# Optimization experiments

Hardware: AMD Instinct MI355X
Metric: run time of the kernel (lower is better)

The kernel has to match this reference:

```python
import jax, jax.numpy as jnp
import numpy as np

H = 56; W = 56; WS = 7; SS = 3; HEADS = 12; DIM = 384
N = WS * WS; NW = (H // WS) * (W // WS); EPS = 1e-5


def _attn_mask():
    img = np.zeros((H, W), np.float32)
    cnt = 0
    for hs in (slice(0, -WS), slice(-WS, -SS), slice(-SS, None)):
        for ws in (slice(0, -WS), slice(-WS, -SS), slice(-SS, None)):
            img[hs, ws] = cnt
            cnt += 1
    m = img.reshape(H // WS, WS, W // WS, WS).transpose(0, 2, 1, 3).reshape(-1, N)
    d = m[:, None, :] - m[:, :, None]
    return jnp.asarray(np.where(d != 0, -100.0, 0.0).astype(np.float32))


def _rel_coords():
    c = np.stack(np.meshgrid(np.arange(WS), np.arange(WS), indexing='ij')).reshape(2, -1)
    rel = (c[:, :, None] - c[:, None, :]).astype(np.float32)
    rel = np.sign(rel) * np.log1p(np.abs(rel))
    return jnp.asarray(np.stack([rel[0], rel[1]], -1).reshape(-1, 2))


ATTN_MASK = _attn_mask()  # (NW, N, N)
REL = _rel_coords()       # (N*N, 2)


def _ln(x, g, b):
    mu = x.mean(-1, keepdims=True)
    var = ((x - mu) ** 2).mean(-1, keepdims=True)
    return (x - mu) / jnp.sqrt(var + EPS) * g + b


def setup_inputs() -> dict:
    key = jax.random.key(0)
    ks = jax.random.split(key, 8)
    s = 0.02
    B = 32
    return {
        'x': jax.random.normal(ks[0], (B, H * W, DIM), jnp.float32),
        'norm1_g': jnp.ones((DIM,), jnp.float32),
        'norm1_b': jnp.zeros((DIM,), jnp.float32),
        'qkv_w': jax.random.normal(ks[1], (DIM, 3 * DIM), jnp.float32) * s,
        'qkv_b': jnp.zeros((3 * DIM,), jnp.float32),
        'tau': jnp.ones((HEADS,), jnp.float32),
        'proj_w': jax.random.normal(ks[2], (DIM, DIM), jnp.float32) * s,
        'proj_b': jnp.zeros((DIM,), jnp.float32),
        'crpb_w1': jax.random.normal(ks[3], (2, 64), jnp.float32) * s,
        'crpb_b1': jnp.zeros((64,), jnp.float32),
        'crpb_w2': jax.random.normal(ks[4], (64, HEADS), jnp.float32) * s,
        'crpb_b2': jnp.zeros((HEADS,), jnp.float32),
        'norm2_g': jnp.ones((DIM,), jnp.float32),
        'norm2_b': jnp.zeros((DIM,), jnp.float32),
        'mlp_w1': jax.random.normal(ks[5], (DIM, 4 * DIM), jnp.float32) * s,
        'mlp_b1': jnp.zeros((4 * DIM,), jnp.float32),
        'mlp_w2': jax.random.normal(ks[6], (4 * DIM, DIM), jnp.float32) * s,
        'mlp_b2': jnp.zeros((DIM,), jnp.float32),
    }


def reference(x, norm1_g, norm1_b, qkv_w, qkv_b, tau, proj_w, proj_b,
              crpb_w1, crpb_b1, crpb_w2, crpb_b2, norm2_g, norm2_b,
              mlp_w1, mlp_b1, mlp_w2, mlp_b2):
    B = x.shape[0]
    shortcut = x
    h = _ln(x, norm1_g, norm1_b).reshape(B, H, W, DIM)
    # cyclic shift
    h = jnp.roll(h, (-SS, -SS), axis=(1, 2))
    # window partition -> (B*NW, N, DIM)
    xw = h.reshape(B, H // WS, WS, W // WS, WS, DIM).transpose(0, 1, 3, 2, 4, 5).reshape(-1, N, DIM)
    qkv = xw @ qkv_w + qkv_b
    q, k, v = jnp.split(qkv, 3, axis=-1)
    hd = DIM // HEADS
    def to_heads(t):
        return t.reshape(-1, N, HEADS, hd).transpose(0, 2, 1, 3)  # (Bw, heads, N, hd)
    q, k, v = to_heads(q), to_heads(k), to_heads(v)
    q = q / jnp.maximum(jnp.linalg.norm(q, axis=-1, keepdims=True), 1e-12)
    k = k / jnp.maximum(jnp.linalg.norm(k, axis=-1, keepdims=True), 1e-12)
    attn = jnp.einsum('whnd,whmd->whnm', q, k) * tau[None, :, None, None]
    # continuous relative position bias
    bias = jax.nn.relu(REL @ crpb_w1 + crpb_b1) @ crpb_w2 + crpb_b2  # (N*N, heads)
    bias = bias.reshape(N, N, HEADS).transpose(2, 0, 1)
    attn = attn + bias[None]
    attn = attn.reshape(B, NW, HEADS, N, N) + ATTN_MASK[None, :, None]
    attn = jax.nn.softmax(attn.reshape(-1, HEADS, N, N), axis=-1)
    out = jnp.einsum('whnm,whmd->whnd', attn, v).transpose(0, 2, 1, 3).reshape(-1, N, DIM)
    out = out @ proj_w + proj_b
    # window reverse
    h = out.reshape(B, H // WS, W // WS, WS, WS, DIM).transpose(0, 1, 3, 2, 4, 5).reshape(B, H, W, DIM)
    h = jnp.roll(h, (SS, SS), axis=(1, 2)).reshape(B, H * W, DIM)
    x = shortcut + h
    m = _ln(x, norm2_g, norm2_b)
    m = jax.nn.gelu(m @ mlp_w1 + mlp_b1, approximate=False) @ mlp_w2 + mlp_b2
    return x + m
```

## Files before the change

kernel.cpp:

```cpp
#include <hip/hip_runtime.h>
#include <cstdint>
#include <cstddef>


typedef unsigned short u16;
typedef __bf16 bf16x8 __attribute__((ext_vector_type(8)));
typedef float f32x4 __attribute__((ext_vector_type(4)));

__device__ __forceinline__ u16 f2bf(float f) {
  unsigned u = __builtin_bit_cast(unsigned, f);
  u += 0x7fffu + ((u >> 16) & 1u);
  return (u16)(u >> 16);
}

__device__ __forceinline__ void gll16(const u16* g, u16* l) {
  __builtin_amdgcn_global_load_lds(
      (const __attribute__((address_space(1))) void*)g,
      (__attribute__((address_space(3))) void*)l, 16, 0, 0);
}

__device__ __forceinline__ bf16x8 ldfrag(const u16* rowp, int l4) {
  return *(const bf16x8*)(rowp + 8 * l4);
}

__global__ __launch_bounds__(256) void fill_k(float* o, int n) {
  int i = blockIdx.x * 256 + threadIdx.x;
  if (i < n) o[i] = 12345.0f;
}

__global__ __launch_bounds__(256) void wconv_k(
    const float* __restrict__ qkv_w, const float* __restrict__ proj_w,
    const float* __restrict__ mlp_w1, const float* __restrict__ mlp_w2,
    u16* __restrict__ o) {
  const int id = blockIdx.x * 256 + threadIdx.x;
  if (id < 442368) {
    const int n = id / 384, k = id - n * 384;
    o[id] = f2bf(qkv_w[k * 1152 + n]);
  } else if (id < 589824) {
    const int e = id - 442368; const int n = e / 384, k = e - n * 384;
    o[id] = f2bf(proj_w[k * 384 + n]);
  } else if (id < 1179648) {
    const int e = id - 589824; const int n = e / 384, k = e - n * 384;
    o[id] = f2bf(mlp_w1[k * 1536 + n]);
  } else {
    const int e = id - 1179648; const int n = e / 1536, k = e - n * 1536;
    o[id] = f2bf(mlp_w2[k * 384 + n]);
  }
}

__global__ __launch_bounds__(256) void biastab_k(
    const float* __restrict__ w1, const float* __restrict__ b1,
    const float* __restrict__ w2, const float* __restrict__ b2,
    float* __restrict__ biasT) {
  const int id = blockIdx.x * 256 + threadIdx.x;
  if (id >= 2401) return;
  const int i = id / 49, j = id - i * 49;
  const int r1 = i / 7, c1 = i - r1 * 7, r2 = j / 7, c2 = j - r2 * 7;
  float dy = (float)(r1 - r2), dx = (float)(c1 - c2);
  dy = copysignf(log1pf(fabsf(dy)), dy);
  dx = copysignf(log1pf(fabsf(dx)), dx);
  float accv[12];
#pragma unroll
  for (int t = 0; t < 12; ++t) accv[t] = b2[t];
  for (int u = 0; u < 64; ++u) {
    float hu = fmaxf(dy * w1[u] + dx * w1[64 + u] + b1[u], 0.0f);
#pragma unroll
    for (int t = 0; t < 12; ++t) accv[t] += hu * w2[u * 12 + t];
  }
#pragma unroll
  for (int t = 0; t < 12; ++t) biasT[t * 2401 + id] = accv[t];
}

template <int WINMAP>
__global__ __launch_bounds__(256, 4) void ln_k(
    const float* __restrict__ X, const float* __restrict__ g,
    const float* __restrict__ b, u16* __restrict__ O) {
  const int t = blockIdx.x * 4 + (threadIdx.x >> 6);
  const int lane = threadIdx.x & 63;
  const float* xr = X + (size_t)t * 384;
  float v[6];
  float s = 0.f;
#pragma unroll
  for (int i = 0; i < 6; ++i) { v[i] = xr[lane + i * 64]; s += v[i]; }
#pragma unroll
  for (int m = 1; m < 64; m <<= 1) s += __shfl_xor(s, m);
  const float mu = s * (1.0f / 384.0f);
  float q = 0.f;
#pragma unroll
  for (int i = 0; i < 6; ++i) { float d = v[i] - mu; q += d * d; }
#pragma unroll
  for (int m = 1; m < 64; m <<= 1) q += __shfl_xor(q, m);
  const float rstd = rsqrtf(q * (1.0f / 384.0f) + 1e-5f);
  size_t row;
  if constexpr (WINMAP) {
    const int bb = t / 3136, hw = t - bb * 3136;
    const int ho = hw / 56, wo = hw - ho * 56;
    int hs = ho - 3; if (hs < 0) hs += 56;
    int ws2 = wo - 3; if (ws2 < 0) ws2 += 56;
    const int h7 = hs / 7, w7 = ws2 / 7;
    const int wwin = bb * 64 + h7 * 8 + w7;
    const int p = (hs - h7 * 7) * 7 + (ws2 - w7 * 7);
    row = (size_t)wwin * 49 + p;
  } else {
    row = (size_t)t;
  }
  u16* orow = O + row * 384;
#pragma unroll
  for (int i = 0; i < 6; ++i) {
    const int d = lane + i * 64;
    orow[d] = f2bf((v[i] - mu) * rstd * g[d] + b[d]);
  }
}

template <int EPI>
__global__ __launch_bounds__(256, 2) void gemm_k(
    const u16* __restrict__ A, const u16* __restrict__ Bt,
    const float* __restrict__ bias, const float* __restrict__ aux,
    void* __restrict__ outp, int M, int N, int K) {
  __shared__ u16 Ash[128 * 32];
  __shared__ u16 Bsh[128 * 32];
  const int tid = threadIdx.x;
  const int lane = tid & 63;
  const int wv = tid >> 6;
  const int wrow = wv >> 1, wcol = wv & 1;
  const int l15 = lane & 15, l4 = lane >> 4;

  const int nx = gridDim.x;
  const int nwg = nx * gridDim.y;
  int bid = blockIdx.y * nx + blockIdx.x;
  bid = (bid & 7) * (nwg >> 3) + (bid >> 3);
  const int tileN = (bid % nx) * 128;
  const int tileM = (bid / nx) * 128;

  f32x4 acc[4][4] = {};

  const int r0 = wv * 16 + (lane >> 2);
  const int c0 = (lane & 3) * 8;
  const u16* Ag = A + (size_t)(tileM + r0) * K + c0;
  const u16* Bg = Bt + (size_t)(tileN + r0) * K + c0;
  const size_t rowskip = (size_t)64 * K;
  u16* Al0 = &Ash[wv * 512];
  u16* Al1 = &Ash[(4 + wv) * 512];
  u16* Bl0 = &Bsh[wv * 512];
  u16* Bl1 = &Bsh[(4 + wv) * 512];

  for (int k0 = 0; k0 < K; k0 += 32) {
    __syncthreads();
    gll16(Ag + k0, Al0);
    gll16(Ag + rowskip + k0, Al1);
    gll16(Bg + k0, Bl0);
    gll16(Bg + rowskip + k0, Bl1);
    __syncthreads();
    bf16x8 af[4], bfr[4];
#pragma unroll
    for (int f = 0; f < 4; ++f) {
      af[f] = ldfrag(&Ash[(wrow * 64 + f * 16 + l15) * 32], l4);
      bfr[f] = ldfrag(&Bsh[(wcol * 64 + f * 16 + l15) * 32], l4);
    }
#pragma unroll
    for (int fm = 0; fm < 4; ++fm)
#pragma unroll
      for (int fn = 0; fn < 4; ++fn)
        acc[fm][fn] = __builtin_amdgcn_mfma_f32_16x16x32_bf16(
            af[fm], bfr[fn], acc[fm][fn], 0, 0, 0);
  }

  const int baseRow = tileM + wrow * 64;
  const int baseCol = tileN + wcol * 64;

  if constexpr (EPI == 0) {
    u16* O = (u16*)outp;
#pragma unroll
    for (int fm = 0; fm < 4; ++fm) {
#pragma unroll
      for (int hp = 0; hp < 2; ++hp) {
        const int c0e = baseCol + hp * 32;
        const int seg = c0e >> 5;
        const bool nrm = seg < 24;
        const float tfac = (seg < 12) ? aux[seg] : 1.0f;
        const float b0 = bias[c0e + l15];
        const float b1 = bias[c0e + 16 + l15];
#pragma unroll
        for (int r = 0; r < 4; ++r) {
          float v0 = acc[fm][2 * hp][r] + b0;
          float v1 = acc[fm][2 * hp + 1][r] + b1;
          if (nrm) {
            float ss = v0 * v0 + v1 * v1;
            ss += __shfl_xor(ss, 1);
            ss += __shfl_xor(ss, 2);
            ss += __shfl_xor(ss, 4);
            ss += __shfl_xor(ss, 8);
            const float f = tfac / fmaxf(sqrtf(ss), 1e-12f);
            v0 *= f; v1 *= f;
          }
          const size_t row = (size_t)(baseRow + fm * 16 + l4 * 4 + r);
          O[row * N + c0e + l15] = f2bf(v0);
          O[row * N + c0e + 16 + l15] = f2bf(v1);
        }
      }
    }
  } else if constexpr (EPI == 1) {
    float* O = (float*)outp;
    const float* X = aux;
#pragma unroll
    for (int fm = 0; fm < 4; ++fm) {
#pragma unroll
      for (int r = 0; r < 4; ++r) {
        const int row = baseRow + fm * 16 + l4 * 4 + r;
        const int w = row / 49, p = row - w * 49;
        const int bb = w >> 6, widx = w & 63;
        const int p7 = p / 7;
        int hs = (widx >> 3) * 7 + p7;
        int ws2 = (widx & 7) * 7 + (p - p7 * 7);
        int ho = hs + 3; if (ho >= 56) ho -= 56;
        int wo = ws2 + 3; if (wo >= 56) wo -= 56;
        const size_t tok = (size_t)bb * 3136 + ho * 56 + wo;
#pragma unroll
        for (int fn = 0; fn < 4; ++fn) {
          const int col = baseCol + fn * 16 + l15;
          O[tok * 384 + col] = X[tok * 384 + col] + acc[fm][fn][r] + bias[col];
        }
      }
    }
  } else if constexpr (EPI == 2) {
    u16* O = (u16*)outp;
#pragma unroll
    for (int fm = 0; fm < 4; ++fm) {
#pragma unroll
      for (int fn = 0; fn < 4; ++fn) {
        const int col = baseCol + fn * 16 + l15;
        const float bc = bias[col];
#pragma unroll
        for (int r = 0; r < 4; ++r) {
          const size_t row = (size_t)(baseRow + fm * 16 + l4 * 4 + r);
          const float v = acc[fm][fn][r] + bc;
          const float g = 0.5f * v * (1.0f + erff(v * 0.70710678118654752f));
          O[row * N + col] = f2bf(g);
        }
      }
    }
  } else {
    float* O = (float*)outp;
#pragma unroll
    for (int fm = 0; fm < 4; ++fm) {
#pragma unroll
      for (int fn = 0; fn < 4; ++fn) {
        const int col = baseCol + fn * 16 + l15;
        const float bc = bias[col];
#pragma unroll
        for (int r = 0; r < 4; ++r) {
          const size_t row = (size_t)(baseRow + fm * 16 + l4 * 4 + r);
          O[row * N + col] += acc[fm][fn][r] + bc;
        }
      }
    }
  }
}

__global__ __launch_bounds__(256, 2) void attn_k(
    const u16* __restrict__ qkv, const float* __restrict__ biasT,
    u16* __restrict__ outp) {
  __shared__ u16 lds[4][7552];
  const int tid = threadIdx.x, lane = tid & 63, wid = tid >> 6;
  const int l15 = lane & 15, l4 = lane >> 4;
  const int W = blockIdx.x * 4 + wid;
  const int w = W / 12, h = W - w * 12;
  u16* S = lds[wid];
  u16* Q = S;
  u16* Kl = S + 2560;
  u16* P = S;
  u16* VT = S + 5120;
  float* sums = (float*)(S + 7424);
  const u16* base = qkv + (size_t)w * 56448 + h * 32;
  const int widx = w & 63, wh = widx >> 3, ww = widx & 7;
  const bool masked = (wh == 7) || (ww == 7);

#pragma unroll
  for (int it = 0; it < 4; ++it) {
    const int row = it * 16 + (lane >> 2);
    const int c8 = (lane & 3) * 8;
    uint4 qv = {0, 0, 0, 0}, kv = {0, 0, 0, 0};
    if (row < 49) {
      qv = *(const uint4*)(base + (size_t)row * 1152 + c8);
      kv = *(const uint4*)(base + (size_t)row * 1152 + 384 + c8);
    }
    *(uint4*)&Q[row * 40 + c8] = qv;
    *(uint4*)&Kl[row * 40 + c8] = kv;
  }
  {
    const int d = lane & 31;
    const int jh = lane >> 5;
#pragma unroll 4
    for (int jt = 0; jt < 32; ++jt) {
      const int j = jt * 2 + jh;
      u16 val = 0;
      if (j < 49) val = base[(size_t)j * 1152 + 768 + d];
      VT[d * 72 + j] = val;
    }
  }
  __syncthreads();

  f32x4 sc[4][4] = {};
  {
    bf16x8 aq[4], bk[4];
#pragma unroll
    for (int f = 0; f < 4; ++f) aq[f] = ldfrag(&Q[(f * 16 + l15) * 40], l4);
#pragma unroll
    for (int f = 0; f < 4; ++f) bk[f] = ldfrag(&Kl[(f * 16 + l15) * 40], l4);
#pragma unroll
    for (int fm = 0; fm < 4; ++fm)
#pragma unroll
      for (int fn = 0; fn < 4; ++fn)
        sc[fm][fn] = __builtin_amdgcn_mfma_f32_16x16x32_bf16(
            aq[fm], bk[fn], sc[fm][fn], 0, 0, 0);
  }
  __syncthreads();

  int codej[4] = {0, 0, 0, 0};
  if (masked) {
#pragma unroll
    for (int fn = 0; fn < 4; ++fn) {
      const int j = fn * 16 + l15;
      const int pr = j / 7, pc = j - pr * 7;
      const int rr2 = (wh == 7) ? ((pr < 4) ? 1 : 2) : 0;
      const int cc2 = (ww == 7) ? ((pc < 4) ? 1 : 2) : 0;
      codej[fn] = rr2 * 3 + cc2;
    }
  }
#pragma unroll
  for (int fm = 0; fm < 4; ++fm) {
#pragma unroll
    for (int r = 0; r < 4; ++r) {
      const int i = fm * 16 + l4 * 4 + r;
      const bool iok = i < 49;
      int ci = 0;
      if (masked && iok) {
        const int pr = i / 7, pc = i - pr * 7;
        const int rr2 = (wh == 7) ? ((pr < 4) ? 1 : 2) : 0;
        const int cc2 = (ww == 7) ? ((pc < 4) ? 1 : 2) : 0;
        ci = rr2 * 3 + cc2;
      }
      const float* brow = biasT + (size_t)h * 2401 + (iok ? i : 0) * 49;
      float sv[4];
#pragma unroll
      for (int fn = 0; fn < 4; ++fn) {
        const int j = fn * 16 + l15;
        float s = sc[fm][fn][r];
        if (iok && j < 49) {
          s += brow[j];
          if (masked && codej[fn] != ci) s -= 100.0f;
        } else {
          s = -1e30f;
        }
        sv[fn] = s;
      }
      float mx = fmaxf(fmaxf(sv[0], sv[1]), fmaxf(sv[2], sv[3]));
      mx = fmaxf(mx, __shfl_xor(mx, 1));
      mx = fmaxf(mx, __shfl_xor(mx, 2));
      mx = fmaxf(mx, __shfl_xor(mx, 4));
      mx = fmaxf(mx, __shfl_xor(mx, 8));
      float sm = 0.f;
      u16 pb[4];
#pragma unroll
      for (int fn = 0; fn < 4; ++fn) {
        const float e = __expf(sv[fn] - mx);
        sm += e;
        pb[fn] = f2bf(e);
      }
      sm += __shfl_xor(sm, 1);
      sm += __shfl_xor(sm, 2);
      sm += __shfl_xor(sm, 4);
      sm += __shfl_xor(sm, 8);
#pragma unroll
      for (int fn = 0; fn < 4; ++fn) P[i * 72 + fn * 16 + l15] = pb[fn];
      if (l15 == 0) sums[i] = sm;
    }
  }
  __syncthreads();

  f32x4 o[4][2] = {};
#pragma unroll
  for (int kk = 0; kk < 2; ++kk) {
    bf16x8 pa[4], bv[2];
#pragma unroll
    for (int fm = 0; fm < 4; ++fm)
      pa[fm] = ldfrag(&P[(fm * 16 + l15) * 72 + kk * 32], l4);
#pragma unroll
    for (int fn = 0; fn < 2; ++fn)
      bv[fn] = ldfrag(&VT[(fn * 16 + l15) * 72 + kk * 32], l4);
#pragma unroll
    for (int fm = 0; fm < 4; ++fm)
#pragma unroll
      for (int fn = 0; fn < 2; ++fn)
        o[fm][fn] = __builtin_amdgcn_mfma_f32_16x16x32_bf16(
            pa[fm], bv[fn], o[fm][fn], 0, 0, 0);
  }
  u16* ob = outp + (size_t)w * 49 * 384 + h * 32;
#pragma unroll
  for (int fm = 0; fm < 4; ++fm) {
#pragma unroll
    for (int r = 0; r < 4; ++r) {
      const int i = fm * 16 + l4 * 4 + r;
      if (i < 49) {
        const float inv = 1.0f / sums[i];
        ob[(size_t)i * 384 + l15] = f2bf(o[fm][0][r] * inv);
        ob[(size_t)i * 384 + 16 + l15] = f2bf(o[fm][1][r] * inv);
      }
    }
  }
}

extern "C" void kernel_launch(void* const* d_in, const int* in_sizes, int n_in,
                              void* d_out, int out_size, void* d_ws,
                              size_t ws_size, hipStream_t stream) {
  const float* x      = (const float*)d_in[0];
  const float* n1g    = (const float*)d_in[1];
  const float* n1b    = (const float*)d_in[2];
  const float* qkv_w  = (const float*)d_in[3];
  const float* qkv_b  = (const float*)d_in[4];
  const float* tau    = (const float*)d_in[5];
  const float* proj_w = (const float*)d_in[6];
  const float* proj_b = (const float*)d_in[7];
  const float* c_w1   = (const float*)d_in[8];
  const float* c_b1   = (const float*)d_in[9];
  const float* c_w2   = (const float*)d_in[10];
  const float* c_b2   = (const float*)d_in[11];
  const float* n2g    = (const float*)d_in[12];
  const float* n2b    = (const float*)d_in[13];
  const float* mlp_w1 = (const float*)d_in[14];
  const float* mlp_b1 = (const float*)d_in[15];
  const float* mlp_w2 = (const float*)d_in[16];
  const float* mlp_b2 = (const float*)d_in[17];
  float* out = (float*)d_out;
  char* ws = (char*)d_ws;

  constexpr size_t WS_WT    = 0;
  constexpr size_t WS_BIAST = 3538944;
  constexpr size_t WS_XW    = 4194304;
  constexpr size_t WS_QKV   = 81264640;
  constexpr size_t WS_ATT   = 312475648;
  constexpr size_t WS_NEED  = 389545984;

  if (ws_size < WS_NEED) {
    fill_k<<<(out_size + 255) / 256, 256, 0, stream>>>(out, out_size);
    return;
  }

  u16* wqkvT  = (u16*)(ws + WS_WT);
  u16* wprojT = (u16*)(ws + WS_WT + 884736);
  u16* wm1T   = (u16*)(ws + WS_WT + 1179648);
  u16* wm2T   = (u16*)(ws + WS_WT + 2359296);
  float* biasT = (float*)(ws + WS_BIAST);
  u16* xw  = (u16*)(ws + WS_XW);
  u16* qkv = (u16*)(ws + WS_QKV);
  u16* att = (u16*)(ws + WS_ATT);
  u16* hid = qkv;
  u16* ln2 = xw;

  wconv_k<<<6912, 256, 0, stream>>>(qkv_w, proj_w, mlp_w1, mlp_w2, (u16*)ws);
  biastab_k<<<10, 256, 0, stream>>>(c_w1, c_b1, c_w2, c_b2, biasT);
  ln_k<1><<<25088, 256, 0, stream>>>(x, n1g, n1b, xw);
  gemm_k<0><<<dim3(9, 784), 256, 0, stream>>>(xw, wqkvT, qkv_b, tau, qkv,
                                              100352, 1152, 384);
  attn_k<<<6144, 256, 0, stream>>>(qkv, biasT, att);
  gemm_k<1><<<dim3(3, 784), 256, 0, stream>>>(att, wprojT, proj_b, x, out,
                                              100352, 384, 384);
  ln_k<0><<<25088, 256, 0, stream>>>(out, n2g, n2b, ln2);
  gemm_k<2><<<dim3(12, 784), 256, 0, stream>>>(ln2, wm1T, mlp_b1, nullptr, hid,
                                               100352, 1536, 384);
  gemm_k<3><<<dim3(3, 784), 256, 0, stream>>>(hid, wm2T, mlp_b2, nullptr, out,
                                              100352, 384, 1536);
}
```

Before: 1.383 ms.

## Rework GEMM into single-wave double-buffered swizzled tiles; drop attention block barriers

The GEMM kernel moves from a 256-thread, 128x128 tile with two barriers per k-step to a 64-thread, 64x64 tile per workgroup. Loads are double-buffered through global_load_lds, gated by explicit vmcnt/lgkmcnt waits, and LDS is XOR-swizzled to avoid bank conflicts. MFMA sections are wrapped in s_setprio. In the attention kernel each wave uses its own LDS slice, so the __syncthreads calls become lgkmcnt waits. The aim is to overlap global loads with MFMA and remove barrier stalls, at the cost of less cross-wave operand reuse in LDS and more global reads per output tile.

```diff
diff --git a/kernel.cpp b/kernel.cpp
--- a/kernel.cpp
+++ b/kernel.cpp
@@ -6,6 +6,10 @@
 typedef unsigned short u16;
 typedef __bf16 bf16x8 __attribute__((ext_vector_type(8)));
 typedef float f32x4 __attribute__((ext_vector_type(4)));
+
+#define VMW8 asm volatile("s_waitcnt vmcnt(8)" ::: "memory")
+#define VMW0 asm volatile("s_waitcnt vmcnt(0)" ::: "memory")
+#define LGKM0 asm volatile("s_waitcnt lgkmcnt(0)" ::: "memory")
 
 __device__ __forceinline__ u16 f2bf(float f) {
   unsigned u = __builtin_bit_cast(unsigned, f);
@@ -17,10 +21,6 @@
   __builtin_amdgcn_global_load_lds(
       (const __attribute__((address_space(1))) void*)g,
       (__attribute__((address_space(3))) void*)l, 16, 0, 0);
-}
-
-__device__ __forceinline__ bf16x8 ldfrag(const u16* rowp, int l4) {
-  return *(const bf16x8*)(rowp + 8 * l4);
 }
 
 __global__ __launch_bounds__(256) void fill_k(float* o, int n) {
@@ -113,60 +113,71 @@
 }
 
 template <int EPI>
-__global__ __launch_bounds__(256, 2) void gemm_k(
+__global__ __launch_bounds__(64, 2) void gemm_k(
     const u16* __restrict__ A, const u16* __restrict__ Bt,
     const float* __restrict__ bias, const float* __restrict__ aux,
     void* __restrict__ outp, int M, int N, int K) {
-  __shared__ u16 Ash[128 * 32];
-  __shared__ u16 Bsh[128 * 32];
-  const int tid = threadIdx.x;
-  const int lane = tid & 63;
-  const int wv = tid >> 6;
-  const int wrow = wv >> 1, wcol = wv & 1;
+  __shared__ u16 Abuf[2][2048];
+  __shared__ u16 Bbuf[2][2048];
+  const int lane = threadIdx.x;
   const int l15 = lane & 15, l4 = lane >> 4;
 
   const int nx = gridDim.x;
   const int nwg = nx * gridDim.y;
   int bid = blockIdx.y * nx + blockIdx.x;
   bid = (bid & 7) * (nwg >> 3) + (bid >> 3);
-  const int tileN = (bid % nx) * 128;
-  const int tileM = (bid / nx) * 128;
+  const int tileN = (bid % nx) * 64;
+  const int tileM = (bid / nx) * 64;
+
+  const int prow_l = lane >> 2;
+  const int lrow_l = prow_l ^ ((prow_l >> 2) & 1);
+  const int lslot = (lane & 3) ^ (lrow_l & 3);
+  const u16* Ag = A + (size_t)(tileM + lrow_l) * K + lslot * 8;
+  const u16* Bg = Bt + (size_t)(tileN + lrow_l) * K + lslot * 8;
+  const size_t cstrideA = (size_t)16 * K;
 
   f32x4 acc[4][4] = {};
 
-  const int r0 = wv * 16 + (lane >> 2);
-  const int c0 = (lane & 3) * 8;
-  const u16* Ag = A + (size_t)(tileM + r0) * K + c0;
-  const u16* Bg = Bt + (size_t)(tileN + r0) * K + c0;
-  const size_t rowskip = (size_t)64 * K;
-  u16* Al0 = &Ash[wv * 512];
-  u16* Al1 = &Ash[(4 + wv) * 512];
-  u16* Bl0 = &Bsh[wv * 512];
-  u16* Bl1 = &Bsh[(4 + wv) * 512];
-
-  for (int k0 = 0; k0 < K; k0 += 32) {
-    __syncthreads();
-    gll16(Ag + k0, Al0);
-    gll16(Ag + rowskip + k0, Al1);
-    gll16(Bg + k0, Bl0);
-    gll16(Bg + rowskip + k0, Bl1);
-    __syncthreads();
-    bf16x8 af[4], bfr[4];
-#pragma unroll
-    for (int f = 0; f < 4; ++f) {
-      af[f] = ldfrag(&Ash[(wrow * 64 + f * 16 + l15) * 32], l4);
-      bfr[f] = ldfrag(&Bsh[(wcol * 64 + f * 16 + l15) * 32], l4);
-    }
-#pragma unroll
-    for (int fm = 0; fm < 4; ++fm)
-#pragma unroll
-      for (int fn = 0; fn < 4; ++fn)
-        acc[fm][fn] = __builtin_amdgcn_mfma_f32_16x16x32_bf16(
-            af[fm], bfr[fn], acc[fm][fn], 0, 0, 0);
-  }
-
-  const int baseRow = tileM + wrow * 64;
-  const int baseCol = tileN + wcol * 64;
+#define STAGE(k0, b)                                             \
+  {                                                              \
+    _Pragma("unroll") for (int c = 0; c < 4; ++c) {              \
+      gll16(Ag + (size_t)c * cstrideA + (k0), &Abuf[b][c * 512]);\
+      gll16(Bg + (size_t)c * cstrideA + (k0), &Bbuf[b][c * 512]);\
+    }                                                            \
+  }
+
+#define COMPUTE(b)                                                        \
+  {                                                                       \
+    bf16x8 af[4], bfr[4];                                                 \
+    _Pragma("unroll") for (int f = 0; f < 4; ++f) {                       \
+      const int R = f * 16 + l15;                                         \
+      const int off = (R * 32 + 8 * l4) ^ ((R & 7) << 3);                 \
+      af[f] = *(const bf16x8*)&Abuf[b][off];                              \
+      bfr[f] = *(const bf16x8*)&Bbuf[b][off];                             \
+    }                                                                     \
+    __builtin_amdgcn_s_setprio(1);                                        \
+    _Pragma("unroll") for (int fm = 0; fm < 4; ++fm)                      \
+        _Pragma("unroll") for (int fn = 0; fn < 4; ++fn) acc[fm][fn] =    \
+            __builtin_amdgcn_mfma_f32_16x16x32_bf16(af[fm], bfr[fn],      \
+                                                    acc[fm][fn], 0, 0, 0);\
+    __builtin_amdgcn_s_setprio(0);                                        \
+  }
+
+  const int nt = K >> 5;
+  STAGE(0, 0);
+  STAGE(32, 1);
+  for (int t = 0; t + 2 < nt; ++t) {
+    VMW8;
+    COMPUTE(t & 1);
+    LGKM0;
+    STAGE((size_t)(t + 2) * 32, t & 1);
+  }
+  VMW8;
+  COMPUTE(nt & 1);
+  VMW0;
+  COMPUTE((nt - 1) & 1);
+#undef STAGE
+#undef COMPUTE
 
   if constexpr (EPI == 0) {
     u16* O = (u16*)outp;
@@ -174,7 +185,7 @@
     for (int fm = 0; fm < 4; ++fm) {
 #pragma unroll
       for (int hp = 0; hp < 2; ++hp) {
-        const int c0e = baseCol + hp * 32;
+        const int c0e = tileN + hp * 32;
         const int seg = c0e >> 5;
         const bool nrm = seg < 24;
         const float tfac = (seg < 12) ? aux[seg] : 1.0f;
@@ -193,7 +204,7 @@
             const float f = tfac / fmaxf(sqrtf(ss), 1e-12f);
             v0 *= f; v1 *= f;
           }
-          const size_t row = (size_t)(baseRow + fm * 16 + l4 * 4 + r);
+          const size_t row = (size_t)(tileM + fm * 16 + l4 * 4 + r);
           O[row * N + c0e + l15] = f2bf(v0);
           O[row * N + c0e + 16 + l15] = f2bf(v1);
         }
@@ -206,7 +217,7 @@
     for (int fm = 0; fm < 4; ++fm) {
 #pragma unroll
       for (int r = 0; r < 4; ++r) {
-        const int row = baseRow + fm * 16 + l4 * 4 + r;
+        const int row = tileM + fm * 16 + l4 * 4 + r;
         const int w = row / 49, p = row - w * 49;
         const int bb = w >> 6, widx = w & 63;
         const int p7 = p / 7;
@@ -217,7 +228,7 @@
         const size_t tok = (size_t)bb * 3136 + ho * 56 + wo;
 #pragma unroll
         for (int fn = 0; fn < 4; ++fn) {
-          const int col = baseCol + fn * 16 + l15;
+          const int col = tileN + fn * 16 + l15;
           O[tok * 384 + col] = X[tok * 384 + col] + acc[fm][fn][r] + bias[col];
         }
       }
@@ -228,11 +239,11 @@
     for (int fm = 0; fm < 4; ++fm) {
 #pragma unroll
       for (int fn = 0; fn < 4; ++fn) {
-        const int col = baseCol + fn * 16 + l15;
+        const int col = tileN + fn * 16 + l15;
         const float bc = bias[col];
 #pragma unroll
         for (int r = 0; r < 4; ++r) {
-          const size_t row = (size_t)(baseRow + fm * 16 + l4 * 4 + r);
+          const size_t row = (size_t)(tileM + fm * 16 + l4 * 4 + r);
           const float v = acc[fm][fn][r] + bc;
           const float g = 0.5f * v * (1.0f + erff(v * 0.70710678118654752f));
           O[row * N + col] = f2bf(g);
@@ -245,11 +256,11 @@
     for (int fm = 0; fm < 4; ++fm) {
 #pragma unroll
       for (int fn = 0; fn < 4; ++fn) {
-        const int col = baseCol + fn * 16 + l15;
+        const int col = tileN + fn * 16 + l15;
         const float bc = bias[col];
 #pragma unroll
         for (int r = 0; r < 4; ++r) {
-          const size_t row = (size_t)(baseRow + fm * 16 + l4 * 4 + r);
+          const size_t row = (size_t)(tileM + fm * 16 + l4 * 4 + r);
           O[row * N + col] += acc[fm][fn][r] + bc;
         }
       }
@@ -298,23 +309,27 @@
       VT[d * 72 + j] = val;
     }
   }
-  __syncthreads();
+  LGKM0;
 
   f32x4 sc[4][4] = {};
   {
     bf16x8 aq[4], bk[4];
 #pragma unroll
-    for (int f = 0; f < 4; ++f) aq[f] = ldfrag(&Q[(f * 16 + l15) * 40], l4);
-#pragma unroll
-    for (int f = 0; f < 4; ++f) bk[f] = ldfrag(&Kl[(f * 16 + l15) * 40], l4);
+    for (int f = 0; f < 4; ++f)
+      aq[f] = *(const bf16x8*)&Q[(f * 16 + l15) * 40 + 8 * l4];
+#pragma unroll
+    for (int f = 0; f < 4; ++f)
+      bk[f] = *(const bf16x8*)&Kl[(f * 16 + l15) * 40 + 8 * l4];
+    __builtin_amdgcn_s_setprio(1);
 #pragma unroll
     for (int fm = 0; fm < 4; ++fm)
 #pragma unroll
       for (int fn = 0; fn < 4; ++fn)
         sc[fm][fn] = __builtin_amdgcn_mfma_f32_16x16x32_bf16(
             aq[fm], bk[fn], sc[fm][fn], 0, 0, 0);
-  }
-  __syncthreads();
+    __builtin_amdgcn_s_setprio(0);
+  }
+  LGKM0;
 
   int codej[4] = {0, 0, 0, 0};
   if (masked) {
@@ -376,7 +391,7 @@
       if (l15 == 0) sums[i] = sm;
     }
   }
-  __syncthreads();
+  LGKM0;
 
   f32x4 o[4][2] = {};
 #pragma unroll
@@ -384,16 +399,18 @@
     bf16x8 pa[4], bv[2];
 #pragma unroll
     for (int fm = 0; fm < 4; ++fm)
-      pa[fm] = ldfrag(&P[(fm * 16 + l15) * 72 + kk * 32], l4);
+      pa[fm] = *(const bf16x8*)&P[(fm * 16 + l15) * 72 + kk * 32 + 8 * l4];
 #pragma unroll
     for (int fn = 0; fn < 2; ++fn)
-      bv[fn] = ldfrag(&VT[(fn * 16 + l15) * 72 + kk * 32], l4);
+      bv[fn] = *(const bf16x8*)&VT[(fn * 16 + l15) * 72 + kk * 32 + 8 * l4];
+    __builtin_amdgcn_s_setprio(1);
 #pragma unroll
     for (int fm = 0; fm < 4; ++fm)
 #pragma unroll
       for (int fn = 0; fn < 2; ++fn)
         o[fm][fn] = __builtin_amdgcn_mfma_f32_16x16x32_bf16(
             pa[fm], bv[fn], o[fm][fn], 0, 0, 0);
+    __builtin_amdgcn_s_setprio(0);
   }
   u16* ob = outp + (size_t)w * 49 * 384 + h * 32;
 #pragma unroll
@@ -460,14 +477,14 @@
   wconv_k<<<6912, 256, 0, stream>>>(qkv_w, proj_w, mlp_w1, mlp_w2, (u16*)ws);
   biastab_k<<<10, 256, 0, stream>>>(c_w1, c_b1, c_w2, c_b2, biasT);
   ln_k<1><<<25088, 256, 0, stream>>>(x, n1g, n1b, xw);
-  gemm_k<0><<<dim3(9, 784), 256, 0, stream>>>(xw, wqkvT, qkv_b, tau, qkv,
-                                              100352, 1152, 384);
+  gemm_k<0><<<dim3(18, 1568), 64, 0, stream>>>(xw, wqkvT, qkv_b, tau, qkv,
+                                               100352, 1152, 384);
   attn_k<<<6144, 256, 0, stream>>>(qkv, biasT, att);
-  gemm_k<1><<<dim3(3, 784), 256, 0, stream>>>(att, wprojT, proj_b, x, out,
+  gemm_k<1><<<dim3(6, 1568), 64, 0, stream>>>(att, wprojT, proj_b, x, out,
                                               100352, 384, 384);
   ln_k<0><<<25088, 256, 0, stream>>>(out, n2g, n2b, ln2);
-  gemm_k<2><<<dim3(12, 784), 256, 0, stream>>>(ln2, wm1T, mlp_b1, nullptr, hid,
+  gemm_k<2><<<dim3(24, 1568), 64, 0, stream>>>(ln2, wm1T, mlp_b1, nullptr, hid,
                                                100352, 1536, 384);
-  gemm_k<3><<<dim3(3, 784), 256, 0, stream>>>(hid, wm2T, mlp_b2, nullptr, out,
+  gemm_k<3><<<dim3(6, 1568), 64, 0, stream>>>(hid, wm2T, mlp_b2, nullptr, out,
                                               100352, 384, 1536);
 }
```

Measured after the change: 1.729 ms. +25.0%, slower.
